# Kernel optimization log

Hardware: AMD Instinct MI355X
Metric: run time of the kernel (lower is better)

Reference implementation:

```python
import jax, jax.numpy as jnp
import numpy as np

B = 64
H = W = 512          # source and target grid size
P = 8                # patch_size
HP = H // P          # 64 patches per side
NP = HP * HP         # 4096 patches
S = P * P            # source_patch_size = 64
TPH = H // HP        # target_patch_h = 8
TPW = W // HP        # target_patch_w = 8
T = TPH * TPW        # target_patch_size = 64


def _gaussian_transforms(init_std=0.1, init_mean=1.0):
    # coords over a PxP patch, row-major (matches torch meshgrid 'ij' + view(-1,2))
    ii, jj = jnp.meshgrid(jnp.arange(P, dtype=jnp.float32),
                          jnp.arange(P, dtype=jnp.float32), indexing='ij')
    coords = jnp.stack([ii.reshape(-1), jj.reshape(-1)], axis=-1)  # [S,2]
    dist_sq = ((coords[:, None, :] - coords[None, :, :]) ** 2).sum(-1)  # [S,S]
    std = P * init_std
    kernel = jnp.exp(-dist_sq / (2.0 * std * std))
    kernel = kernel - kernel.mean() + init_mean
    return jnp.broadcast_to(kernel[None], (NP, T, S)).copy()  # [NP,T,S] (T==S here)


def setup_inputs() -> dict:
    key = jax.random.key(0)
    k1, k2 = jax.random.split(key)
    src = jax.random.uniform(k1, (B, H, W), dtype=jnp.float32)
    transforms = _gaussian_transforms()
    gates = jax.random.normal(k2, (NP,), dtype=jnp.float32) * 0.01 + 1.0
    biases = jnp.zeros((NP,), dtype=jnp.float32)
    return {"src": src, "transforms": transforms, "gates": gates, "biases": biases}


def reference(src, transforms, gates, biases):
    # unfold (non-overlapping, stride == kernel): [B,H,W] -> [B, NP, S]
    patches = (src.reshape(B, HP, P, HP, P)
                  .transpose(0, 1, 3, 2, 4)
                  .reshape(B, NP, S))
    # per-patch batched matmul: bps,pts->bpt
    X = jnp.einsum('bps,pts->bpt', patches, transforms)
    # gate / bias / activity mask
    strength = patches.sum(axis=-1, keepdims=True)          # [B,NP,1]
    mask = (strength > 0).astype(X.dtype)
    final = (X * gates[None, :, None] + biases[None, :, None]) * mask  # [B,NP,T]
    # fold: [B,NP,T] -> [B, target_h, target_w]
    out = (final.reshape(B, HP, HP, TPH, TPW)
                .transpose(0, 1, 3, 2, 4)
                .reshape(B, HP * TPH, HP * TPW))
    return out
```

## Files before the change

### kernel.cpp

```cpp
#include <hip/hip_runtime.h>

#define HW 512

typedef __attribute__((ext_vector_type(4))) float f32x4;
typedef __attribute__((ext_vector_type(8))) short b16x8;
typedef __attribute__((ext_vector_type(4))) short b16x4;

__device__ __forceinline__ short f2bf(float f) {
    union { float f; unsigned u; } v; v.f = f;
    return (short)((v.u + 0x7FFFu + ((v.u >> 16) & 1u)) >> 16);
}

__global__ __launch_bounds__(512, 4) void axonal_kernel(
    const float* __restrict__ src, const float* __restrict__ tr,
    const float* __restrict__ gates, const float* __restrict__ biases,
    float* __restrict__ out)
{
    const int gi  = blockIdx.x;
    const int ph  = gi >> 3;
    const int pwg = gi & 7;
    const int tid = threadIdx.x;
    const int w   = tid >> 6;
    const int lane = tid & 63;
    const int lo  = lane & 15;
    const int hi  = lane >> 4;
    const int p   = (ph << 6) + (pwg << 3) + w;

    __shared__ __align__(16) short pbuf[16 * 520];
    __shared__ __align__(16) float obuf[16 * 548];
    __shared__ __align__(16) float smask[128];

    b16x8 bfr[8];
    {
        const float* tp = tr + ((size_t)p << 12);
        #pragma unroll
        for (int n = 0; n < 4; ++n)
            #pragma unroll
            for (int ks = 0; ks < 2; ++ks) {
                const float* rp = tp + (n * 16 + lo) * 64 + ks * 32 + 4 * hi;
                float4 u0 = *reinterpret_cast<const float4*>(rp);
                float4 u1 = *reinterpret_cast<const float4*>(rp + 16);
                b16x8 v;
                v[0] = f2bf(u0.x); v[1] = f2bf(u0.y); v[2] = f2bf(u0.z); v[3] = f2bf(u0.w);
                v[4] = f2bf(u1.x); v[5] = f2bf(u1.y); v[6] = f2bf(u1.z); v[7] = f2bf(u1.w);
                bfr[n * 2 + ks] = v;
            }
    }
    const float g  = gates[p];
    const float bi = biases[p];

    const int sb   = tid >> 5;
    const int sp   = (tid >> 2) & 7;
    const int ssub = tid & 3;
    const float* sbase = src + (size_t)(ph * 8 + 2 * ssub) * HW + pwg * 64 + sp * 8;

    float4 ld0, ld1, ld2, ld3;
    {
        const float* q = sbase + (size_t)sb * HW * HW;
        ld0 = *reinterpret_cast<const float4*>(q);
        ld1 = *reinterpret_cast<const float4*>(q + 4);
        ld2 = *reinterpret_cast<const float4*>(q + HW);
        ld3 = *reinterpret_cast<const float4*>(q + HW + 4);
    }

    for (int c = 0; c < 4; ++c) {
        float s = (ld0.x + ld0.y + ld0.z + ld0.w) + (ld1.x + ld1.y + ld1.z + ld1.w)
                + (ld2.x + ld2.y + ld2.z + ld2.w) + (ld3.x + ld3.y + ld3.z + ld3.w);
        s += __shfl_xor(s, 1);
        s += __shfl_xor(s, 2);
        if (ssub == 0) smask[sp * 16 + sb] = s;

        b16x8 w0, w1;
        w0[0] = f2bf(ld0.x); w0[1] = f2bf(ld0.y); w0[2] = f2bf(ld0.z); w0[3] = f2bf(ld0.w);
        w0[4] = f2bf(ld1.x); w0[5] = f2bf(ld1.y); w0[6] = f2bf(ld1.z); w0[7] = f2bf(ld1.w);
        w1[0] = f2bf(ld2.x); w1[1] = f2bf(ld2.y); w1[2] = f2bf(ld2.z); w1[3] = f2bf(ld2.w);
        w1[4] = f2bf(ld3.x); w1[5] = f2bf(ld3.y); w1[6] = f2bf(ld3.z); w1[7] = f2bf(ld3.w);
        short* dst = &pbuf[sb * 520 + sp * 64 + ssub * 16];
        *reinterpret_cast<b16x8*>(dst)     = w0;
        *reinterpret_cast<b16x8*>(dst + 8) = w1;
        __syncthreads();

        if (c < 3) {
            const float* q = sbase + (size_t)((c + 1) * 16 + sb) * HW * HW;
            ld0 = *reinterpret_cast<const float4*>(q);
            ld1 = *reinterpret_cast<const float4*>(q + 4);
            ld2 = *reinterpret_cast<const float4*>(q + HW);
            ld3 = *reinterpret_cast<const float4*>(q + HW + 4);
        }

        f32x4 acc[4];
        acc[0] = (f32x4){0.f, 0.f, 0.f, 0.f};
        acc[1] = acc[0]; acc[2] = acc[0]; acc[3] = acc[0];
        #pragma unroll
        for (int ks = 0; ks < 2; ++ks) {
            const short* ap = &pbuf[lo * 520 + w * 64 + ks * 32 + 4 * hi];
            b16x4 a0 = *reinterpret_cast<const b16x4*>(ap);
            b16x4 a1 = *reinterpret_cast<const b16x4*>(ap + 16);
            b16x8 a;
            a[0] = a0[0]; a[1] = a0[1]; a[2] = a0[2]; a[3] = a0[3];
            a[4] = a1[0]; a[5] = a1[1]; a[6] = a1[2]; a[7] = a1[3];
            acc[0] = __builtin_amdgcn_mfma_f32_16x16x32_bf16(a, bfr[0 + ks], acc[0], 0, 0, 0);
            acc[1] = __builtin_amdgcn_mfma_f32_16x16x32_bf16(a, bfr[2 + ks], acc[1], 0, 0, 0);
            acc[2] = __builtin_amdgcn_mfma_f32_16x16x32_bf16(a, bfr[4 + ks], acc[2], 0, 0, 0);
            acc[3] = __builtin_amdgcn_mfma_f32_16x16x32_bf16(a, bfr[6 + ks], acc[3], 0, 0, 0);
        }

        f32x4 mk = *reinterpret_cast<const f32x4*>(&smask[w * 16 + 4 * hi]);
        #pragma unroll
        for (int n = 0; n < 4; ++n) {
            const int t = n * 16 + lo;
            float* ob = &obuf[(t >> 3) * 68 + w * 8 + (t & 7)];
            #pragma unroll
            for (int q = 0; q < 4; ++q) {
                float val = fmaf(acc[n][q], g, bi);
                val = (mk[q] > 0.f) ? val : 0.f;
                ob[(4 * hi + q) * 548] = val;
            }
        }
        __syncthreads();

        #pragma unroll
        for (int i = 0; i < 4; ++i) {
            const int flat = i * 512 + tid;
            const int f4 = flat & 15, r = (flat >> 4) & 7, b = flat >> 7;
            float4 v = *reinterpret_cast<const float4*>(&obuf[b * 548 + r * 68 + f4 * 4]);
            *reinterpret_cast<float4*>(out + (size_t)(c * 16 + b) * HW * HW
                + (size_t)(ph * 8 + r) * HW + pwg * 64 + f4 * 4) = v;
        }
    }
}

extern "C" void kernel_launch(void* const* d_in, const int* in_sizes, int n_in,
                              void* d_out, int out_size, void* d_ws, size_t ws_size,
                              hipStream_t stream) {
    const float* src    = (const float*)d_in[0];
    const float* tr     = (const float*)d_in[1];
    const float* gates  = (const float*)d_in[2];
    const float* biases = (const float*)d_in[3];
    float* out = (float*)d_out;

    dim3 grid(512);
    dim3 block(512);
    hipLaunchKernelGGL(axonal_kernel, grid, block, 0, stream,
                       src, tr, gates, biases, out);
}
```

Baseline: 37.80 us.

## Split work into smaller blocks of 4 patches and 32 batches, store outputs directly

Reorganizes the grid from 512 blocks of 512 threads into 2048 blocks of 256 threads. Each block now covers 4 patches and 32 batch items, loading all source data up front with a single sync. The LDS staging buffer and second barrier for the output are removed, so MFMA results go straight to global memory as scalar strided stores. This adds parallelism and removes sync and LDS traffic. In exchange, each block loads its transform fragments with less reuse (32 batches instead of 64), and the output writes are uncoalesced scalar stores.

```diff
diff --git a/kernel.cpp b/kernel.cpp
--- a/kernel.cpp
+++ b/kernel.cpp
@@ -1,6 +1,7 @@
 #include <hip/hip_runtime.h>
 
 #define HW 512
+#define BSTRIDE 268
 
 typedef __attribute__((ext_vector_type(4))) float f32x4;
 typedef __attribute__((ext_vector_type(8))) short b16x8;
@@ -11,24 +12,24 @@
     return (short)((v.u + 0x7FFFu + ((v.u >> 16) & 1u)) >> 16);
 }
 
-__global__ __launch_bounds__(512, 4) void axonal_kernel(
+__global__ __launch_bounds__(256, 6) void axonal_kernel(
     const float* __restrict__ src, const float* __restrict__ tr,
     const float* __restrict__ gates, const float* __restrict__ biases,
     float* __restrict__ out)
 {
     const int gi  = blockIdx.x;
-    const int ph  = gi >> 3;
-    const int pwg = gi & 7;
+    const int pq  = gi & 15;
+    const int ph  = (gi >> 4) & 63;
+    const int bh  = gi >> 10;
     const int tid = threadIdx.x;
     const int w   = tid >> 6;
     const int lane = tid & 63;
     const int lo  = lane & 15;
     const int hi  = lane >> 4;
-    const int p   = (ph << 6) + (pwg << 3) + w;
+    const int p   = (ph << 6) + (pq << 2) + w;
 
-    __shared__ __align__(16) short pbuf[16 * 520];
-    __shared__ __align__(16) float obuf[16 * 548];
-    __shared__ __align__(16) float smask[128];
+    __shared__ __align__(16) short pbuf[32 * BSTRIDE];
+    __shared__ __align__(16) float smask[4 * 32];
 
     b16x8 bfr[8];
     {
@@ -49,83 +50,56 @@
     const float g  = gates[p];
     const float bi = biases[p];
 
-    const int sb   = tid >> 5;
-    const int sp   = (tid >> 2) & 7;
-    const int ssub = tid & 3;
-    const float* sbase = src + (size_t)(ph * 8 + 2 * ssub) * HW + pwg * 64 + sp * 8;
+    {
+        const int sb = tid >> 3;
+        const int u  = tid & 7;
+        const float* sp = src + (size_t)(bh * 32 + sb) * HW * HW
+                              + (size_t)(ph * 8) * HW + pq * 32 + u * 4;
+        short* dst = &pbuf[sb * BSTRIDE + (u >> 1) * 64 + (u & 1) * 4];
+        float ssum = 0.f;
+        #pragma unroll
+        for (int r = 0; r < 8; ++r) {
+            float4 v = *reinterpret_cast<const float4*>(sp + r * HW);
+            ssum += (v.x + v.y) + (v.z + v.w);
+            b16x4 bv;
+            bv[0] = f2bf(v.x); bv[1] = f2bf(v.y); bv[2] = f2bf(v.z); bv[3] = f2bf(v.w);
+            *reinterpret_cast<b16x4*>(dst + r * 8) = bv;
+        }
+        ssum += __shfl_xor(ssum, 1);
+        if ((u & 1) == 0) smask[(u >> 1) * 32 + sb] = ssum;
+    }
+    __syncthreads();
 
-    float4 ld0, ld1, ld2, ld3;
-    {
-        const float* q = sbase + (size_t)sb * HW * HW;
-        ld0 = *reinterpret_cast<const float4*>(q);
-        ld1 = *reinterpret_cast<const float4*>(q + 4);
-        ld2 = *reinterpret_cast<const float4*>(q + HW);
-        ld3 = *reinterpret_cast<const float4*>(q + HW + 4);
-    }
-
-    for (int c = 0; c < 4; ++c) {
-        float s = (ld0.x + ld0.y + ld0.z + ld0.w) + (ld1.x + ld1.y + ld1.z + ld1.w)
-                + (ld2.x + ld2.y + ld2.z + ld2.w) + (ld3.x + ld3.y + ld3.z + ld3.w);
-        s += __shfl_xor(s, 1);
-        s += __shfl_xor(s, 2);
-        if (ssub == 0) smask[sp * 16 + sb] = s;
-
-        b16x8 w0, w1;
-        w0[0] = f2bf(ld0.x); w0[1] = f2bf(ld0.y); w0[2] = f2bf(ld0.z); w0[3] = f2bf(ld0.w);
-        w0[4] = f2bf(ld1.x); w0[5] = f2bf(ld1.y); w0[6] = f2bf(ld1.z); w0[7] = f2bf(ld1.w);
-        w1[0] = f2bf(ld2.x); w1[1] = f2bf(ld2.y); w1[2] = f2bf(ld2.z); w1[3] = f2bf(ld2.w);
-        w1[4] = f2bf(ld3.x); w1[5] = f2bf(ld3.y); w1[6] = f2bf(ld3.z); w1[7] = f2bf(ld3.w);
-        short* dst = &pbuf[sb * 520 + sp * 64 + ssub * 16];
-        *reinterpret_cast<b16x8*>(dst)     = w0;
-        *reinterpret_cast<b16x8*>(dst + 8) = w1;
-        __syncthreads();
-
-        if (c < 3) {
-            const float* q = sbase + (size_t)((c + 1) * 16 + sb) * HW * HW;
-            ld0 = *reinterpret_cast<const float4*>(q);
-            ld1 = *reinterpret_cast<const float4*>(q + 4);
-            ld2 = *reinterpret_cast<const float4*>(q + HW);
-            ld3 = *reinterpret_cast<const float4*>(q + HW + 4);
-        }
-
-        f32x4 acc[4];
-        acc[0] = (f32x4){0.f, 0.f, 0.f, 0.f};
-        acc[1] = acc[0]; acc[2] = acc[0]; acc[3] = acc[0];
+    #pragma unroll
+    for (int bg = 0; bg < 2; ++bg) {
+        f32x4 acc0 = (f32x4){0.f, 0.f, 0.f, 0.f};
+        f32x4 acc1 = acc0, acc2 = acc0, acc3 = acc0;
         #pragma unroll
         for (int ks = 0; ks < 2; ++ks) {
-            const short* ap = &pbuf[lo * 520 + w * 64 + ks * 32 + 4 * hi];
+            const short* ap = &pbuf[(bg * 16 + lo) * BSTRIDE + w * 64 + ks * 32 + 4 * hi];
             b16x4 a0 = *reinterpret_cast<const b16x4*>(ap);
             b16x4 a1 = *reinterpret_cast<const b16x4*>(ap + 16);
             b16x8 a;
             a[0] = a0[0]; a[1] = a0[1]; a[2] = a0[2]; a[3] = a0[3];
             a[4] = a1[0]; a[5] = a1[1]; a[6] = a1[2]; a[7] = a1[3];
-            acc[0] = __builtin_amdgcn_mfma_f32_16x16x32_bf16(a, bfr[0 + ks], acc[0], 0, 0, 0);
-            acc[1] = __builtin_amdgcn_mfma_f32_16x16x32_bf16(a, bfr[2 + ks], acc[1], 0, 0, 0);
-            acc[2] = __builtin_amdgcn_mfma_f32_16x16x32_bf16(a, bfr[4 + ks], acc[2], 0, 0, 0);
-            acc[3] = __builtin_amdgcn_mfma_f32_16x16x32_bf16(a, bfr[6 + ks], acc[3], 0, 0, 0);
+            acc0 = __builtin_amdgcn_mfma_f32_16x16x32_bf16(a, bfr[0 + ks], acc0, 0, 0, 0);
+            acc1 = __builtin_amdgcn_mfma_f32_16x16x32_bf16(a, bfr[2 + ks], acc1, 0, 0, 0);
+            acc2 = __builtin_amdgcn_mfma_f32_16x16x32_bf16(a, bfr[4 + ks], acc2, 0, 0, 0);
+            acc3 = __builtin_amdgcn_mfma_f32_16x16x32_bf16(a, bfr[6 + ks], acc3, 0, 0, 0);
         }
 
-        f32x4 mk = *reinterpret_cast<const f32x4*>(&smask[w * 16 + 4 * hi]);
+        f32x4 mk = *reinterpret_cast<const f32x4*>(&smask[w * 32 + bg * 16 + 4 * hi]);
+        float* ob = out + (size_t)(bh * 32 + bg * 16 + 4 * hi) * HW * HW
+                        + (size_t)(ph * 8 + (lo >> 3)) * HW + pq * 32 + w * 8 + (lo & 7);
         #pragma unroll
         for (int n = 0; n < 4; ++n) {
-            const int t = n * 16 + lo;
-            float* ob = &obuf[(t >> 3) * 68 + w * 8 + (t & 7)];
+            f32x4 acc = (n == 0) ? acc0 : (n == 1) ? acc1 : (n == 2) ? acc2 : acc3;
             #pragma unroll
             for (int q = 0; q < 4; ++q) {
-                float val = fmaf(acc[n][q], g, bi);
+                float val = fmaf(acc[q], g, bi);
                 val = (mk[q] > 0.f) ? val : 0.f;
-                ob[(4 * hi + q) * 548] = val;
+                ob[(size_t)q * HW * HW + (size_t)(2 * n) * HW] = val;
             }
-        }
-        __syncthreads();
-
-        #pragma unroll
-        for (int i = 0; i < 4; ++i) {
-            const int flat = i * 512 + tid;
-            const int f4 = flat & 15, r = (flat >> 4) & 7, b = flat >> 7;
-            float4 v = *reinterpret_cast<const float4*>(&obuf[b * 548 + r * 68 + f4 * 4]);
-            *reinterpret_cast<float4*>(out + (size_t)(c * 16 + b) * HW * HW
-                + (size_t)(ph * 8 + r) * HW + pwg * 64 + f4 * 4) = v;
         }
     }
 }
@@ -139,8 +113,8 @@
     const float* biases = (const float*)d_in[3];
     float* out = (float*)d_out;
 
-    dim3 grid(512);
-    dim3 block(512);
+    dim3 grid(2048);
+    dim3 block(256);
     hipLaunchKernelGGL(axonal_kernel, grid, block, 0, stream,
                        src, tr, gates, biases, out);
 }
```

After: 60.00 us. 58.7% more time.
